# Kernel tuning notes

Measured on AMD Instinct MI355X. Metric: run time of the kernel, lower is better.

Reference implementation:

```python
import jax, jax.numpy as jnp
import numpy as np

HEADS, D_K = 8, 64   # dim=512 -> d_k = dim//heads = 64; with dim_head=64 the rearrange collapses to [B,H,N,d_k]
EPS = 1e-5


def _per_head_layernorm(t, g, b):
    # t: [B,H,N,D]; g,b: [H,D] (independent LayerNorm per head, biased variance like torch)
    mu = t.mean(-1, keepdims=True)
    var = ((t - mu) ** 2).mean(-1, keepdims=True)
    return (t - mu) * jax.lax.rsqrt(var + EPS) * g[None, :, None, :] + b[None, :, None, :]


def setup_inputs() -> dict:
    key = jax.random.key(0)
    k0, k1, k2, k3, k4, k5 = jax.random.split(key, 6)
    B, N, DIM = 4, 2048, 512
    inner = HEADS * D_K  # = DIM here
    x = jax.random.normal(k0, (B, N, DIM), jnp.float32)
    W_qkv = jax.random.normal(k1, (DIM, 3 * inner), jnp.float32) * (DIM ** -0.5)  # xavier-ish, no bias
    g_q = 1.0 + 0.1 * jax.random.normal(k2, (HEADS, D_K), jnp.float32)
    b_q = 0.1 * jax.random.normal(k3, (HEADS, D_K), jnp.float32)
    g_k = 1.0 + 0.1 * jax.random.normal(k4, (HEADS, D_K), jnp.float32)
    b_k = 0.1 * jax.random.normal(k5, (HEADS, D_K), jnp.float32)
    return {"x": x, "W_qkv": W_qkv, "g_q": g_q, "b_q": b_q, "g_k": g_k, "b_k": b_k}


def reference(x, W_qkv, g_q, b_q, g_k, b_k):
    B, N, _ = x.shape
    qkv = x @ W_qkv                              # [B,N,3*H*D]
    q, k, v = jnp.split(qkv, 3, axis=-1)

    def split_heads(t):
        return t.reshape(B, N, HEADS, D_K).transpose(0, 2, 1, 3)  # [B,H,N,D]

    q, k, v = map(split_heads, (q, k, v))
    q = _per_head_layernorm(q, g_q, b_q)
    k = _per_head_layernorm(k, g_k, b_k)
    # un-normalized linear attention: scale by 1/sqrt(d_k) then by 1/seq_len (no softmax)
    dots = jnp.einsum('bhnd,bhmd->bhnm', q, k) * (D_K ** -0.5)
    p_attn = dots / N
    out = jnp.einsum('bhnm,bhmd->bhnd', p_attn, v)  # [B,H,N,D]
    return out.transpose(0, 2, 1, 3).reshape(B, N, HEADS * D_K)
```

## Files before the change

kernel.cpp:

```cpp
#include <hip/hip_runtime.h>
#include <hip/hip_bf16.h>
#include <stdint.h>

using bf16   = __bf16;
using bf16x4 = __attribute__((ext_vector_type(4))) __bf16;
using bf16x8 = __attribute__((ext_vector_type(8))) __bf16;
using f32x4  = __attribute__((ext_vector_type(4))) float;

static constexpr int BATCH = 4, SEQ = 2048, DIM = 512, HEADS = 8, DK = 64;
static constexpr int M    = BATCH * SEQ;
static constexpr int NQKV = 3 * DIM;

#define GLD16(src, dst)                                                        \
    __builtin_amdgcn_global_load_lds(                                          \
        (const __attribute__((address_space(1))) void*)(src),                  \
        (__attribute__((address_space(3))) void*)(dst), 16, 0, 0)

__global__ __launch_bounds__(256) void k_prep(const float* __restrict__ w,
                                              bf16* __restrict__ wt,
                                              float* __restrict__ S)
{
    const int bid = blockIdx.x;
    const int t   = threadIdx.x;
    const int WB  = (DIM / 32) * (NQKV / 32);

    if (bid < WB) {
        const int rt = bid / 48, ct = bid - rt * 48;
        __shared__ float tile[32][33];
        const int r = t >> 5, c = t & 31;
        #pragma unroll
        for (int i = 0; i < 4; ++i)
            tile[r + i * 8][c] = w[(rt * 32 + r + i * 8) * NQKV + ct * 32 + c];
        __syncthreads();
        #pragma unroll
        for (int i = 0; i < 4; ++i)
            wt[(ct * 32 + r + i * 8) * DIM + rt * 32 + c] = (bf16)tile[c][r + i * 8];
    } else {
        const int sb = bid - WB;
        const int i  = (sb * 256 + t) * 4;
        *(f32x4*)(S + i) = (f32x4){0.f, 0.f, 0.f, 0.f};
    }
}

__global__ __launch_bounds__(384) void k_gemm(const float* __restrict__ x,
                                              const bf16* __restrict__ Wt,
                                              const float* __restrict__ gq,
                                              const float* __restrict__ bq,
                                              const float* __restrict__ gk,
                                              const float* __restrict__ bk,
                                              bf16* __restrict__ qn,
                                              float* __restrict__ S)
{
    __shared__ union {
        struct { bf16 A[128 * 64]; bf16 B[192 * 64]; } g;
        struct { bf16 q[2][64][72]; bf16 kst[64 * 128]; bf16 vst[64 * 128]; } e;
    } u;

    const int t    = threadIdx.x;
    const int lane = t & 63, wave = t >> 6;
    const int wm   = wave & 1, ws = wave >> 1;
    const int orig = blockIdx.x;
    const int wg   = (orig & 7) * 64 + (orig >> 3);
    const int mt   = wg >> 3, h = wg & 7;
    const int m0   = mt * 128;

    const int l15 = lane & 15, l4 = lane >> 4;
    const int rl  = lane >> 3, cl = (lane & 7) ^ rl;

    f32x4 acc[4][4] = {};

    for (int k0 = 0; k0 < 512; k0 += 64) {
        #pragma unroll
        for (int i = 0; i < 4; ++i) {
            const int ch  = wave * 4 + i;
            const int sec = ch >> 3;
            const int r   = (ch & 7) * 8 + rl;
            GLD16(Wt + ((sec * 512 + h * 64 + r) * 512 + k0 + cl * 8),
                  u.g.B + ch * 512);
        }
        for (int i = t; i < 2048; i += 384) {
            const int row = i >> 4, ch = i & 15;
            float4 v = *(const float4*)(x + (m0 + row) * 512 + k0 + ch * 4);
            bf16x4 o = { (bf16)v.x, (bf16)v.y, (bf16)v.z, (bf16)v.w };
            *(bf16x4*)(u.g.A + row * 64 + (((ch >> 1) ^ (row & 7)) * 8) + (ch & 1) * 4) = o;
        }
        __syncthreads();
        #pragma unroll
        for (int kh = 0; kh < 2; ++kh) {
            bf16x8 af[4], bfv[4];
            const int rc = kh * 4 + l4;
            #pragma unroll
            for (int mf = 0; mf < 4; ++mf) {
                const int row = wm * 64 + mf * 16 + l15;
                af[mf] = *(const bf16x8*)(u.g.A + row * 64 + ((rc ^ (row & 7)) * 8));
            }
            #pragma unroll
            for (int nf = 0; nf < 4; ++nf) {
                const int row = ws * 64 + nf * 16 + l15;
                bfv[nf] = *(const bf16x8*)(u.g.B + row * 64 + ((rc ^ (row & 7)) * 8));
            }
            #pragma unroll
            for (int mf = 0; mf < 4; ++mf)
                #pragma unroll
                for (int nf = 0; nf < 4; ++nf)
                    acc[mf][nf] = __builtin_amdgcn_mfma_f32_16x16x32_bf16(
                        af[mf], bfv[nf], acc[mf][nf], 0, 0, 0);
        }
        __syncthreads();
    }

    const int b  = m0 >> 11;
    const int bh = b * 8 + h;
    const int nwbase = (m0 & 2047) + wm * 64;

    if (ws < 2) {
        const float* gp = (ws == 0 ? gq : gk) + h * 64;
        const float* bp = (ws == 0 ? bq : bk) + h * 64;
        float gv[4], bv[4];
        #pragma unroll
        for (int nf = 0; nf < 4; ++nf) {
            gv[nf] = gp[nf * 16 + l15];
            bv[nf] = bp[nf * 16 + l15];
        }
        #pragma unroll
        for (int mf = 0; mf < 4; ++mf) {
            float mu[4], rs[4];
            #pragma unroll
            for (int r = 0; r < 4; ++r) {
                float s = 0.f, s2 = 0.f;
                #pragma unroll
                for (int nf = 0; nf < 4; ++nf) {
                    const float xv = acc[mf][nf][r];
                    s += xv; s2 += xv * xv;
                }
                s  += __shfl_xor(s, 1);  s  += __shfl_xor(s, 2);
                s  += __shfl_xor(s, 4);  s  += __shfl_xor(s, 8);
                s2 += __shfl_xor(s2, 1); s2 += __shfl_xor(s2, 2);
                s2 += __shfl_xor(s2, 4); s2 += __shfl_xor(s2, 8);
                mu[r] = s * (1.f / 64.f);
                rs[r] = rsqrtf(s2 * (1.f / 64.f) - mu[r] * mu[r] + 1e-5f);
            }
            #pragma unroll
            for (int nf = 0; nf < 4; ++nf) {
                bf16x4 pk;
                #pragma unroll
                for (int r = 0; r < 4; ++r)
                    pk[r] = (bf16)((acc[mf][nf][r] - mu[r]) * rs[r] * gv[nf] + bv[nf]);
                if (ws == 0) {
                    *(bf16x4*)(&u.e.q[wm][nf * 16 + l15][mf * 16 + l4 * 4]) = pk;
                } else {
                    const int d = nf * 16 + l15;
                    const int c = wm * 8 + mf * 2 + (l4 >> 1);
                    *(bf16x4*)(u.e.kst + d * 128 + ((c ^ (d & 7)) * 8) + (l4 & 1) * 4) = pk;
                }
            }
        }
    } else {
        #pragma unroll
        for (int mf = 0; mf < 4; ++mf)
            #pragma unroll
            for (int nf = 0; nf < 4; ++nf) {
                bf16x4 pk;
                #pragma unroll
                for (int r = 0; r < 4; ++r) pk[r] = (bf16)acc[mf][nf][r];
                const int d = nf * 16 + l15;
                const int c = wm * 8 + mf * 2 + (l4 >> 1);
                *(bf16x4*)(u.e.vst + d * 128 + ((c ^ (d & 7)) * 8) + (l4 & 1) * 4) = pk;
            }
    }

    if (ws == 0) {
        bf16* dst = qn + ((long)bh * SEQ + nwbase) * 64;
        const int nq = lane & 15, dq2 = lane >> 4;
        #pragma unroll
        for (int j = 0; j < 4; ++j) {
            const int d0 = (j * 4 + dq2) * 4;
            bf16x4 a0 = *(const bf16x4*)(&u.e.q[wm][d0 + 0][nq * 4]);
            bf16x4 a1 = *(const bf16x4*)(&u.e.q[wm][d0 + 1][nq * 4]);
            bf16x4 a2 = *(const bf16x4*)(&u.e.q[wm][d0 + 2][nq * 4]);
            bf16x4 a3 = *(const bf16x4*)(&u.e.q[wm][d0 + 3][nq * 4]);
            #pragma unroll
            for (int c = 0; c < 4; ++c) {
                bf16x4 o = { a0[c], a1[c], a2[c], a3[c] };
                *(bf16x4*)(dst + (nq * 4 + c) * 64 + d0) = o;
            }
        }
    }

    __syncthreads();

    if (ws == 2) {
        f32x4 sac[4][4] = {};
        #pragma unroll
        for (int kk = 0; kk < 2; ++kk) {
            const int ksi = wm * 2 + kk;
            const int c   = ksi * 4 + l4;
            bf16x8 av[4], bk8[4];
            #pragma unroll
            for (int i = 0; i < 4; ++i) {
                const int dp = i * 16 + l15;
                av[i] = *(const bf16x8*)(u.e.vst + dp * 128 + ((c ^ (dp & 7)) * 8));
            }
            #pragma unroll
            for (int j = 0; j < 4; ++j) {
                const int dd = j * 16 + l15;
                bk8[j] = *(const bf16x8*)(u.e.kst + dd * 128 + ((c ^ (dd & 7)) * 8));
            }
            #pragma unroll
            for (int i = 0; i < 4; ++i)
                #pragma unroll
                for (int j = 0; j < 4; ++j)
                    sac[i][j] = __builtin_amdgcn_mfma_f32_16x16x32_bf16(
                        av[i], bk8[j], sac[i][j], 0, 0, 0);
        }
        float* Sb = S + bh * 4096;
        #pragma unroll
        for (int i = 0; i < 4; ++i)
            #pragma unroll
            for (int j = 0; j < 4; ++j)
                #pragma unroll
                for (int r = 0; r < 4; ++r) {
                    const int dp = i * 16 + l4 * 4 + r;
                    const int dd = j * 16 + l15;
                    atomicAdd(Sb + dp * 64 + dd, sac[i][j][r]);
                }
    }
}

__global__ __launch_bounds__(256) void k_out(const bf16* __restrict__ qn,
                                             const float* __restrict__ S,
                                             float* __restrict__ out)
{
    const int bid = blockIdx.x;
    const int bh = bid >> 3, nt = bid & 7;
    const int b = bh >> 3, h = bh & 7;
    const int t = threadIdx.x, lane = t & 63, wave = t >> 6;
    const int l15 = lane & 15, l4 = lane >> 4;
    const float* Sb = S + bh * 4096;

    bf16x8 bfr[2][4];
    #pragma unroll
    for (int kh = 0; kh < 2; ++kh)
        #pragma unroll
        for (int cf = 0; cf < 4; ++cf) {
            const float* p = Sb + (cf * 16 + l15) * 64 + kh * 32 + l4 * 8;
            float4 lo = *(const float4*)(p);
            float4 hi = *(const float4*)(p + 4);
            bf16x8 f;
            f[0] = (bf16)lo.x; f[1] = (bf16)lo.y; f[2] = (bf16)lo.z; f[3] = (bf16)lo.w;
            f[4] = (bf16)hi.x; f[5] = (bf16)hi.y; f[6] = (bf16)hi.z; f[7] = (bf16)hi.w;
            bfr[kh][cf] = f;
        }

    const bf16* qb = qn + (long)bh * SEQ * 64;
    const int nbase = nt * 256 + wave * 64;
    const float scale = 1.f / 16384.f;

    #pragma unroll
    for (int mf = 0; mf < 4; ++mf) {
        bf16x8 a0 = *(const bf16x8*)(qb + (nbase + mf * 16 + l15) * 64 +      l4 * 8);
        bf16x8 a1 = *(const bf16x8*)(qb + (nbase + mf * 16 + l15) * 64 + 32 + l4 * 8);
        f32x4 acc[4] = {};
        #pragma unroll
        for (int cf = 0; cf < 4; ++cf) {
            acc[cf] = __builtin_amdgcn_mfma_f32_16x16x32_bf16(a0, bfr[0][cf], acc[cf], 0, 0, 0);
            acc[cf] = __builtin_amdgcn_mfma_f32_16x16x32_bf16(a1, bfr[1][cf], acc[cf], 0, 0, 0);
        }
        #pragma unroll
        for (int cf = 0; cf < 4; ++cf)
            #pragma unroll
            for (int r = 0; r < 4; ++r) {
                const int n = nbase + mf * 16 + l4 * 4 + r;
                out[((long)b * SEQ + n) * 512 + h * 64 + cf * 16 + l15] = acc[cf][r] * scale;
            }
    }
}

extern "C" void kernel_launch(void* const* d_in, const int* in_sizes, int n_in,
                              void* d_out, int out_size, void* d_ws, size_t ws_size,
                              hipStream_t stream)
{
    const float* x  = (const float*)d_in[0];
    const float* w  = (const float*)d_in[1];
    const float* gq = (const float*)d_in[2];
    const float* bq = (const float*)d_in[3];
    const float* gk = (const float*)d_in[4];
    const float* bk = (const float*)d_in[5];
    float* out = (float*)d_out;

    char* ws = (char*)d_ws;
    bf16*  wt = (bf16*)(ws);
    bf16*  qn = (bf16*)(ws + 1572864);
    float* S  = (float*)(ws + 9961472);

    hipLaunchKernelGGL(k_prep, dim3(768 + 128), dim3(256), 0, stream, w, wt, S);
    hipLaunchKernelGGL(k_gemm, dim3(512), dim3(384), 0, stream,
                       x, wt, gq, bq, gk, bk, qn, S);
    hipLaunchKernelGGL(k_out,  dim3(256), dim3(256), 0, stream, qn, S, out);
}
```

Baseline: 125.5 us.

## Pre-convert x to bf16 and double-buffer GEMM LDS staging with async loads

The fp32-to-bf16 conversion of x moves into the prep kernel, so the GEMM can stage both A and B tiles with direct global-to-LDS loads into double-buffered shared memory, overlapping the next k-tile's fetch with the current MFMAs. The output kernel folds the scale into S before the bf16 conversion and uses twice as many blocks, each handling half the rows. In exchange, x is written and read back as an extra 8 MB bf16 buffer, and GEMM shared memory roughly doubles, which may lower occupancy.

```diff
diff --git a/kernel.cpp b/kernel.cpp
--- a/kernel.cpp
+++ b/kernel.cpp
@@ -16,16 +16,25 @@
         (const __attribute__((address_space(1))) void*)(src),                  \
         (__attribute__((address_space(3))) void*)(dst), 16, 0, 0)
 
-__global__ __launch_bounds__(256) void k_prep(const float* __restrict__ w,
+__global__ __launch_bounds__(256) void k_prep(const float* __restrict__ x,
+                                              const float* __restrict__ w,
+                                              bf16* __restrict__ xbf,
                                               bf16* __restrict__ wt,
                                               float* __restrict__ S)
 {
     const int bid = blockIdx.x;
     const int t   = threadIdx.x;
+    const int XB  = (M * DIM) / (256 * 4);
     const int WB  = (DIM / 32) * (NQKV / 32);
 
-    if (bid < WB) {
-        const int rt = bid / 48, ct = bid - rt * 48;
+    if (bid < XB) {
+        const int i = (bid * 256 + t) * 4;
+        float4 v = *(const float4*)(x + i);
+        bf16x4 o = { (bf16)v.x, (bf16)v.y, (bf16)v.z, (bf16)v.w };
+        *(bf16x4*)(xbf + i) = o;
+    } else if (bid < XB + WB) {
+        const int wb = bid - XB;
+        const int rt = wb / 48, ct = wb - rt * 48;
         __shared__ float tile[32][33];
         const int r = t >> 5, c = t & 31;
         #pragma unroll
@@ -36,13 +45,13 @@
         for (int i = 0; i < 4; ++i)
             wt[(ct * 32 + r + i * 8) * DIM + rt * 32 + c] = (bf16)tile[c][r + i * 8];
     } else {
-        const int sb = bid - WB;
+        const int sb = bid - XB - WB;
         const int i  = (sb * 256 + t) * 4;
         *(f32x4*)(S + i) = (f32x4){0.f, 0.f, 0.f, 0.f};
     }
 }
 
-__global__ __launch_bounds__(384) void k_gemm(const float* __restrict__ x,
+__global__ __launch_bounds__(384) void k_gemm(const bf16* __restrict__ xbf,
                                               const bf16* __restrict__ Wt,
                                               const float* __restrict__ gq,
                                               const float* __restrict__ bq,
@@ -52,7 +61,7 @@
                                               float* __restrict__ S)
 {
     __shared__ union {
-        struct { bf16 A[128 * 64]; bf16 B[192 * 64]; } g;
+        struct { bf16 A[2][128 * 64]; bf16 B[2][192 * 64]; } g;
         struct { bf16 q[2][64][72]; bf16 kst[64 * 128]; bf16 vst[64 * 128]; } e;
     } u;
 
@@ -67,24 +76,28 @@
     const int l15 = lane & 15, l4 = lane >> 4;
     const int rl  = lane >> 3, cl = (lane & 7) ^ rl;
 
+    auto stage = [&](int buf, int k0) {
+        for (int c = wave; c < 40; c += 6) {
+            if (c < 16) {
+                const int r = c * 8 + rl;
+                GLD16(xbf + (m0 + r) * 512 + k0 + cl * 8, u.g.A[buf] + c * 512);
+            } else {
+                const int ch  = c - 16;
+                const int sec = ch >> 3;
+                const int r   = (ch & 7) * 8 + rl;
+                GLD16(Wt + ((sec * 512 + h * 64 + r) * 512 + k0 + cl * 8),
+                      u.g.B[buf] + ch * 512);
+            }
+        }
+    };
+
     f32x4 acc[4][4] = {};
 
-    for (int k0 = 0; k0 < 512; k0 += 64) {
-        #pragma unroll
-        for (int i = 0; i < 4; ++i) {
-            const int ch  = wave * 4 + i;
-            const int sec = ch >> 3;
-            const int r   = (ch & 7) * 8 + rl;
-            GLD16(Wt + ((sec * 512 + h * 64 + r) * 512 + k0 + cl * 8),
-                  u.g.B + ch * 512);
-        }
-        for (int i = t; i < 2048; i += 384) {
-            const int row = i >> 4, ch = i & 15;
-            float4 v = *(const float4*)(x + (m0 + row) * 512 + k0 + ch * 4);
-            bf16x4 o = { (bf16)v.x, (bf16)v.y, (bf16)v.z, (bf16)v.w };
-            *(bf16x4*)(u.g.A + row * 64 + (((ch >> 1) ^ (row & 7)) * 8) + (ch & 1) * 4) = o;
-        }
-        __syncthreads();
+    stage(0, 0);
+    __syncthreads();
+    int cur = 0;
+    for (int it = 0; it < 8; ++it) {
+        if (it < 7) stage(cur ^ 1, (it + 1) * 64);
         #pragma unroll
         for (int kh = 0; kh < 2; ++kh) {
             bf16x8 af[4], bfv[4];
@@ -92,12 +105,12 @@
             #pragma unroll
             for (int mf = 0; mf < 4; ++mf) {
                 const int row = wm * 64 + mf * 16 + l15;
-                af[mf] = *(const bf16x8*)(u.g.A + row * 64 + ((rc ^ (row & 7)) * 8));
+                af[mf] = *(const bf16x8*)(u.g.A[cur] + row * 64 + ((rc ^ (row & 7)) * 8));
             }
             #pragma unroll
             for (int nf = 0; nf < 4; ++nf) {
                 const int row = ws * 64 + nf * 16 + l15;
-                bfv[nf] = *(const bf16x8*)(u.g.B + row * 64 + ((rc ^ (row & 7)) * 8));
+                bfv[nf] = *(const bf16x8*)(u.g.B[cur] + row * 64 + ((rc ^ (row & 7)) * 8));
             }
             #pragma unroll
             for (int mf = 0; mf < 4; ++mf)
@@ -107,6 +120,7 @@
                         af[mf], bfv[nf], acc[mf][nf], 0, 0, 0);
         }
         __syncthreads();
+        cur ^= 1;
     }
 
     const int b  = m0 >> 11;
@@ -232,11 +246,12 @@
                                              float* __restrict__ out)
 {
     const int bid = blockIdx.x;
-    const int bh = bid >> 3, nt = bid & 7;
+    const int bh = bid >> 4, nt4 = bid & 15;
     const int b = bh >> 3, h = bh & 7;
     const int t = threadIdx.x, lane = t & 63, wave = t >> 6;
     const int l15 = lane & 15, l4 = lane >> 4;
     const float* Sb = S + bh * 4096;
+    const float scale = 1.f / 16384.f;
 
     bf16x8 bfr[2][4];
     #pragma unroll
@@ -247,17 +262,18 @@
             float4 lo = *(const float4*)(p);
             float4 hi = *(const float4*)(p + 4);
             bf16x8 f;
-            f[0] = (bf16)lo.x; f[1] = (bf16)lo.y; f[2] = (bf16)lo.z; f[3] = (bf16)lo.w;
-            f[4] = (bf16)hi.x; f[5] = (bf16)hi.y; f[6] = (bf16)hi.z; f[7] = (bf16)hi.w;
+            f[0] = (bf16)(lo.x * scale); f[1] = (bf16)(lo.y * scale);
+            f[2] = (bf16)(lo.z * scale); f[3] = (bf16)(lo.w * scale);
+            f[4] = (bf16)(hi.x * scale); f[5] = (bf16)(hi.y * scale);
+            f[6] = (bf16)(hi.z * scale); f[7] = (bf16)(hi.w * scale);
             bfr[kh][cf] = f;
         }
 
     const bf16* qb = qn + (long)bh * SEQ * 64;
-    const int nbase = nt * 256 + wave * 64;
-    const float scale = 1.f / 16384.f;
+    const int nbase = nt4 * 128 + wave * 32;
 
     #pragma unroll
-    for (int mf = 0; mf < 4; ++mf) {
+    for (int mf = 0; mf < 2; ++mf) {
         bf16x8 a0 = *(const bf16x8*)(qb + (nbase + mf * 16 + l15) * 64 +      l4 * 8);
         bf16x8 a1 = *(const bf16x8*)(qb + (nbase + mf * 16 + l15) * 64 + 32 + l4 * 8);
         f32x4 acc[4] = {};
@@ -271,7 +287,7 @@
             #pragma unroll
             for (int r = 0; r < 4; ++r) {
                 const int n = nbase + mf * 16 + l4 * 4 + r;
-                out[((long)b * SEQ + n) * 512 + h * 64 + cf * 16 + l15] = acc[cf][r] * scale;
+                out[((long)b * SEQ + n) * 512 + h * 64 + cf * 16 + l15] = acc[cf][r];
             }
     }
 }
@@ -289,12 +305,14 @@
     float* out = (float*)d_out;
 
     char* ws = (char*)d_ws;
-    bf16*  wt = (bf16*)(ws);
-    bf16*  qn = (bf16*)(ws + 1572864);
-    float* S  = (float*)(ws + 9961472);
-
-    hipLaunchKernelGGL(k_prep, dim3(768 + 128), dim3(256), 0, stream, w, wt, S);
+    bf16*  xbf = (bf16*)(ws);
+    bf16*  wt  = (bf16*)(ws + 8388608);
+    bf16*  qn  = (bf16*)(ws + 9961472);
+    float* S   = (float*)(ws + 18350080);
+
+    hipLaunchKernelGGL(k_prep, dim3(4096 + 768 + 128), dim3(256), 0, stream,
+                       x, w, xbf, wt, S);
     hipLaunchKernelGGL(k_gemm, dim3(512), dim3(384), 0, stream,
-                       x, wt, gq, bq, gk, bk, qn, S);
-    hipLaunchKernelGGL(k_out,  dim3(256), dim3(256), 0, stream, qn, S, out);
+                       xbf, wt, gq, bq, gk, bk, qn, S);
+    hipLaunchKernelGGL(k_out,  dim3(512), dim3(256), 0, stream, qn, S, out);
 }
```

Result: slower. 129.3 us (+3.0%).

## Replace global atomic KV-state accumulation with per-tile partials reduced in output kernel

Applied to the files above, without the earlier changes.

Each GEMM workgroup no longer atomically adds its 64x64 K^T V contribution into a shared global S buffer. Its two wave groups now reduce through LDS and write a private partial per (m-tile, head). The output kernel sums the 16 partials per batch-head, stages the result in LDS and folds the scale into the bf16 conversion. This removes atomic contention and the S zeroing in the prep kernel. The cost is more workspace traffic and redundant partial summation in each of the 8 output blocks per batch-head.

```diff
diff --git a/kernel.cpp b/kernel.cpp
--- a/kernel.cpp
+++ b/kernel.cpp
@@ -17,29 +17,20 @@
         (__attribute__((address_space(3))) void*)(dst), 16, 0, 0)
 
 __global__ __launch_bounds__(256) void k_prep(const float* __restrict__ w,
-                                              bf16* __restrict__ wt,
-                                              float* __restrict__ S)
+                                              bf16* __restrict__ wt)
 {
     const int bid = blockIdx.x;
     const int t   = threadIdx.x;
-    const int WB  = (DIM / 32) * (NQKV / 32);
-
-    if (bid < WB) {
-        const int rt = bid / 48, ct = bid - rt * 48;
-        __shared__ float tile[32][33];
-        const int r = t >> 5, c = t & 31;
-        #pragma unroll
-        for (int i = 0; i < 4; ++i)
-            tile[r + i * 8][c] = w[(rt * 32 + r + i * 8) * NQKV + ct * 32 + c];
-        __syncthreads();
-        #pragma unroll
-        for (int i = 0; i < 4; ++i)
-            wt[(ct * 32 + r + i * 8) * DIM + rt * 32 + c] = (bf16)tile[c][r + i * 8];
-    } else {
-        const int sb = bid - WB;
-        const int i  = (sb * 256 + t) * 4;
-        *(f32x4*)(S + i) = (f32x4){0.f, 0.f, 0.f, 0.f};
-    }
+    const int rt = bid / 48, ct = bid - rt * 48;
+    __shared__ float tile[32][33];
+    const int r = t >> 5, c = t & 31;
+    #pragma unroll
+    for (int i = 0; i < 4; ++i)
+        tile[r + i * 8][c] = w[(rt * 32 + r + i * 8) * NQKV + ct * 32 + c];
+    __syncthreads();
+    #pragma unroll
+    for (int i = 0; i < 4; ++i)
+        wt[(ct * 32 + r + i * 8) * DIM + rt * 32 + c] = (bf16)tile[c][r + i * 8];
 }
 
 __global__ __launch_bounds__(384) void k_gemm(const float* __restrict__ x,
@@ -49,7 +40,7 @@
                                               const float* __restrict__ gk,
                                               const float* __restrict__ bk,
                                               bf16* __restrict__ qn,
-                                              float* __restrict__ S)
+                                              float* __restrict__ Sp)
 {
     __shared__ union {
         struct { bf16 A[128 * 64]; bf16 B[192 * 64]; } g;
@@ -213,48 +204,86 @@
                     sac[i][j] = __builtin_amdgcn_mfma_f32_16x16x32_bf16(
                         av[i], bk8[j], sac[i][j], 0, 0, 0);
         }
-        float* Sb = S + bh * 4096;
-        #pragma unroll
-        for (int i = 0; i < 4; ++i)
-            #pragma unroll
-            for (int j = 0; j < 4; ++j)
-                #pragma unroll
-                for (int r = 0; r < 4; ++r) {
-                    const int dp = i * 16 + l4 * 4 + r;
-                    const int dd = j * 16 + l15;
-                    atomicAdd(Sb + dp * 64 + dd, sac[i][j][r]);
-                }
+        float* red = (float*)u.e.q;
+        if (wm == 0) {
+            #pragma unroll
+            for (int i = 0; i < 4; ++i)
+                #pragma unroll
+                for (int j = 0; j < 4; ++j)
+                    *(f32x4*)(red + ((i * 16 + l4 * 4) * 64 + j * 16 + l15) + 0) =
+                        (f32x4){0.f, 0.f, 0.f, 0.f};
+        }
+        if (wm == 0) {
+            #pragma unroll
+            for (int i = 0; i < 4; ++i)
+                #pragma unroll
+                for (int j = 0; j < 4; ++j)
+                    #pragma unroll
+                    for (int r = 0; r < 4; ++r)
+                        red[(i * 16 + l4 * 4 + r) * 64 + j * 16 + l15] = sac[i][j][r];
+        }
+        __builtin_amdgcn_s_barrier();
+        if (wm == 1) {
+            float* Sb = Sp + (long)(mt * 8 + h) * 4096;
+            #pragma unroll
+            for (int i = 0; i < 4; ++i)
+                #pragma unroll
+                for (int j = 0; j < 4; ++j)
+                    #pragma unroll
+                    for (int r = 0; r < 4; ++r) {
+                        const int dp = i * 16 + l4 * 4 + r;
+                        const int dd = j * 16 + l15;
+                        Sb[dp * 64 + dd] = sac[i][j][r] + red[dp * 64 + dd];
+                    }
+        }
     }
 }
 
 __global__ __launch_bounds__(256) void k_out(const bf16* __restrict__ qn,
-                                             const float* __restrict__ S,
+                                             const float* __restrict__ Sp,
                                              float* __restrict__ out)
 {
+    __shared__ float sS[64 * 68];
     const int bid = blockIdx.x;
-    const int bh = bid >> 3, nt = bid & 7;
+    const int bh = bid >> 3, nt8 = bid & 7;
     const int b = bh >> 3, h = bh & 7;
     const int t = threadIdx.x, lane = t & 63, wave = t >> 6;
     const int l15 = lane & 15, l4 = lane >> 4;
-    const float* Sb = S + bh * 4096;
-
+
+    f32x4 racc[4] = {};
+    for (int mt16 = 0; mt16 < 16; ++mt16) {
+        const float* p = Sp + (long)(((b * 16 + mt16) * 8) + h) * 4096 + t * 4;
+        #pragma unroll
+        for (int j = 0; j < 4; ++j)
+            racc[j] += *(const f32x4*)(p + j * 1024);
+    }
+    #pragma unroll
+    for (int j = 0; j < 4; ++j) {
+        const int f  = j * 1024 + t * 4;
+        const int dp = f >> 6, dd = f & 63;
+        *(f32x4*)(sS + dp * 68 + dd) = racc[j];
+    }
+    __syncthreads();
+
+    const float scale = 1.f / 16384.f;
     bf16x8 bfr[2][4];
     #pragma unroll
     for (int kh = 0; kh < 2; ++kh)
         #pragma unroll
         for (int cf = 0; cf < 4; ++cf) {
-            const float* p = Sb + (cf * 16 + l15) * 64 + kh * 32 + l4 * 8;
+            const float* p = sS + (cf * 16 + l15) * 68 + kh * 32 + l4 * 8;
             float4 lo = *(const float4*)(p);
             float4 hi = *(const float4*)(p + 4);
             bf16x8 f;
-            f[0] = (bf16)lo.x; f[1] = (bf16)lo.y; f[2] = (bf16)lo.z; f[3] = (bf16)lo.w;
-            f[4] = (bf16)hi.x; f[5] = (bf16)hi.y; f[6] = (bf16)hi.z; f[7] = (bf16)hi.w;
+            f[0] = (bf16)(lo.x * scale); f[1] = (bf16)(lo.y * scale);
+            f[2] = (bf16)(lo.z * scale); f[3] = (bf16)(lo.w * scale);
+            f[4] = (bf16)(hi.x * scale); f[5] = (bf16)(hi.y * scale);
+            f[6] = (bf16)(hi.z * scale); f[7] = (bf16)(hi.w * scale);
             bfr[kh][cf] = f;
         }
 
     const bf16* qb = qn + (long)bh * SEQ * 64;
-    const int nbase = nt * 256 + wave * 64;
-    const float scale = 1.f / 16384.f;
+    const int nbase = nt8 * 256 + wave * 64;
 
     #pragma unroll
     for (int mf = 0; mf < 4; ++mf) {
@@ -271,7 +300,7 @@
             #pragma unroll
             for (int r = 0; r < 4; ++r) {
                 const int n = nbase + mf * 16 + l4 * 4 + r;
-                out[((long)b * SEQ + n) * 512 + h * 64 + cf * 16 + l15] = acc[cf][r] * scale;
+                out[((long)b * SEQ + n) * 512 + h * 64 + cf * 16 + l15] = acc[cf][r];
             }
     }
 }
@@ -291,10 +320,10 @@
     char* ws = (char*)d_ws;
     bf16*  wt = (bf16*)(ws);
     bf16*  qn = (bf16*)(ws + 1572864);
-    float* S  = (float*)(ws + 9961472);
-
-    hipLaunchKernelGGL(k_prep, dim3(768 + 128), dim3(256), 0, stream, w, wt, S);
+    float* Sp = (float*)(ws + 9961472);
+
+    hipLaunchKernelGGL(k_prep, dim3(768), dim3(256), 0, stream, w, wt);
     hipLaunchKernelGGL(k_gemm, dim3(512), dim3(384), 0, stream,
-                       x, wt, gq, bq, gk, bk, qn, S);
-    hipLaunchKernelGGL(k_out,  dim3(256), dim3(256), 0, stream, qn, S, out);
+                       x, wt, gq, bq, gk, bk, qn, Sp);
+    hipLaunchKernelGGL(k_out,  dim3(256), dim3(256), 0, stream, qn, Sp, out);
 }
```

After: 119.9 us. 1.05x faster.
